# Performance work log

Measured on AMD Instinct MI355X. Metric: run time of the kernel, lower is better.

The kernel has to match this reference:

```python
import jax, jax.numpy as jnp
import numpy as np

B, C_IN, C_OUT, H, W = 128, 128, 128, 40, 40
NUM_EXPERTS, TOP_K, EXPAND = 8, 2, 2
C_HID = C_IN * EXPAND


def setup_inputs() -> dict:
    key = jax.random.key(0)
    ks = jax.random.split(key, 6)
    x = jax.random.normal(ks[0], (B, C_IN, H, W), dtype=jnp.float32)
    weights = jax.random.uniform(ks[1], (B, TOP_K), dtype=jnp.float32)
    indices = jax.random.randint(ks[2], (B, TOP_K), 0, NUM_EXPERTS, dtype=jnp.int64)
    # per-expert 1x1 conv params: expand -> SiLU -> project
    W1 = jax.random.normal(ks[3], (NUM_EXPERTS, C_HID, C_IN), dtype=jnp.float32) * (1.0 / np.sqrt(C_IN))
    b1 = jnp.zeros((NUM_EXPERTS, C_HID), dtype=jnp.float32)
    W2 = jax.random.normal(ks[4], (NUM_EXPERTS, C_OUT, C_HID), dtype=jnp.float32) * (1.0 / np.sqrt(C_HID))
    b2 = jnp.zeros((NUM_EXPERTS, C_OUT), dtype=jnp.float32)
    return {"x": x, "weights": weights, "indices": indices,
            "W1": W1, "b1": b1, "W2": W2, "b2": b2}


def reference(x, weights, indices, W1, b1, W2, b2):
    # Combine top-k gate weights per (batch, expert): duplicate expert picks sum,
    # exactly matching the original's per-expert gather + weighted index_add_.
    Bn = x.shape[0]
    E = W1.shape[0]
    gate = jnp.zeros((Bn, E), dtype=x.dtype).at[jnp.arange(Bn)[:, None], indices].add(weights)  # [B, E]
    out = jnp.zeros((Bn, W2.shape[1]) + x.shape[2:], dtype=x.dtype)
    for e in range(E):  # fixed small expert loop
        h = jax.nn.silu(jnp.einsum('bchw,oc->bohw', x, W1[e]) + b1[e][None, :, None, None])
        y = jnp.einsum('bchw,oc->bohw', h, W2[e]) + b2[e][None, :, None, None]
        out = out + y * gate[:, e][:, None, None, None]
    return out
```

## Files before the change

### kernel.cpp

```cpp
#include <hip/hip_runtime.h>

#define CIN   128
#define CHID  256
#define COUT  128
#define HWPX  1600

typedef __attribute__((ext_vector_type(8))) short bf16x8;
typedef __attribute__((ext_vector_type(4))) float f32x4;

__device__ __forceinline__ unsigned short f2bf(float f) {
  unsigned int u = __builtin_bit_cast(unsigned int, f);
  u += 0x7FFFu + ((u >> 16) & 1u);
  return (unsigned short)(u >> 16);
}
__device__ __forceinline__ unsigned int pack_bf2(float a, float b) {
  return (unsigned int)f2bf(a) | ((unsigned int)f2bf(b) << 16);
}
__device__ __forceinline__ unsigned int silu_gate_pk(float a, float b, float g) {
  const float ea = __builtin_amdgcn_exp2f(a * -1.442695041f);
  const float eb = __builtin_amdgcn_exp2f(b * -1.442695041f);
  const float sa = g * a * __builtin_amdgcn_rcpf(1.0f + ea);
  const float sb = g * b * __builtin_amdgcn_rcpf(1.0f + eb);
  return pack_bf2(sa, sb);
}

__global__ __launch_bounds__(256) void convert_w_kernel(
    const float* __restrict__ W1, const float* __restrict__ W2,
    unsigned short* __restrict__ W1c, unsigned short* __restrict__ W2c) {
  const int i    = blockIdx.x * 256 + threadIdx.x;
  const int j    = i & 7;
  const int lane = (i >> 3) & 63;
  const int r16  = lane & 15;
  const int q    = lane >> 4;
  {
    const int half = (i >> 9) & 1;
    const int ks   = (i >> 10) & 3;
    const int grp  = (i >> 12) & 7;
    const int e    = i >> 15;
    const int ch   = grp * 32 + ((r16 >> 2) << 3) + (r16 & 3) + (half << 2);
    const int c    = ks * 4 + q;
    W1c[i] = f2bf(W1[(e * CHID + ch) * CIN + c * 8 + j]);
  }
  {
    const int mt  = (i >> 9) & 7;
    const int grp = (i >> 12) & 7;
    const int e   = i >> 15;
    const int co  = mt * 16 + r16;
    W2c[i] = f2bf(W2[(e * COUT + co) * CHID + grp * 32 + q * 8 + j]);
  }
}

__global__ __launch_bounds__(256, 2) void moe_kernel(
    const float* __restrict__ x, const float* __restrict__ wts,
    const int* __restrict__ idx, const unsigned short* __restrict__ W1,
    const float* __restrict__ b1, const unsigned short* __restrict__ W2,
    const float* __restrict__ b2, float* __restrict__ out) {
  __shared__ __align__(16) unsigned short lds[32768];

  const int tid  = threadIdx.x;
  const int wave = tid >> 6;
  const int lane = tid & 63;
  const int q    = lane >> 4;
  const int r16  = lane & 15;

  const int  b    = blockIdx.x / 7;
  const int  t4   = blockIdx.x % 7;
  const int  tile = t4 * 4 + wave;
  if (tile >= 25) return;
  const int  px0  = tile * 64;

  unsigned short* xw = &lds[wave * 8192];

  {
    const float* xb = x + (long)b * CIN * HWPX + px0 + lane;
#pragma unroll 4
    for (int c = 0; c < 16; ++c) {
      float v[8];
#pragma unroll
      for (int jj = 0; jj < 8; ++jj) v[jj] = xb[(long)(c * 8 + jj) * HWPX];
      union { bf16x8 w; unsigned int u[4]; } t;
#pragma unroll
      for (int d = 0; d < 4; ++d) t.u[d] = pack_bf2(v[2 * d], v[2 * d + 1]);
      const int slot = (c + lane) & 15;
      *reinterpret_cast<bf16x8*>(&xw[(lane * 16 + slot) * 8]) = t.w;
    }
  }

  const int   e0 = __builtin_amdgcn_readfirstlane(idx[b * 2 + 0]);
  const int   e1 = __builtin_amdgcn_readfirstlane(idx[b * 2 + 1]);
  const float g0 = wts[b * 2 + 0], g1 = wts[b * 2 + 1];

  f32x4 accO[8][4];
#pragma unroll
  for (int mt = 0; mt < 8; ++mt)
#pragma unroll
    for (int nt = 0; nt < 4; ++nt) accO[mt][nt] = (f32x4){0.f, 0.f, 0.f, 0.f};

  const int lane8 = lane * 8;

  for (int gs = 0; gs < 16; ++gs) {
    const int   slot = gs >> 3;
    const int   grp  = gs & 7;
    const int   e    = slot ? e1 : e0;
    const float g    = slot ? g1 : g0;
    const unsigned short* w1s = W1 + ((long)(e * 8 + grp) << 12);
    const unsigned short* w2s = W2 + ((long)(e * 8 + grp) << 12);

    f32x4 aA[4], aB[4];
#pragma unroll
    for (int nt = 0; nt < 4; ++nt) {
      aA[nt] = (f32x4){0.f, 0.f, 0.f, 0.f};
      aB[nt] = (f32x4){0.f, 0.f, 0.f, 0.f};
    }
#pragma unroll
    for (int ks = 0; ks < 4; ++ks) {
      const bf16x8 w0 = *reinterpret_cast<const bf16x8*>(
          &w1s[(ks * 2 + 0) * 512 + lane8]);
      const bf16x8 w1v = *reinterpret_cast<const bf16x8*>(
          &w1s[(ks * 2 + 1) * 512 + lane8]);
#pragma unroll
      for (int nt = 0; nt < 4; ++nt) {
        const int px = nt * 16 + r16;
        const bf16x8 xf = *reinterpret_cast<const bf16x8*>(
            &xw[(px * 16 + ((ks * 4 + q + px) & 15)) * 8]);
        aA[nt] = __builtin_amdgcn_mfma_f32_16x16x32_bf16(w0, xf, aA[nt], 0, 0, 0);
        aB[nt] = __builtin_amdgcn_mfma_f32_16x16x32_bf16(w1v, xf, aB[nt], 0, 0, 0);
      }
    }

    const float* b1e = b1 + e * CHID + grp * 32;
    const f32x4 bA = *reinterpret_cast<const f32x4*>(&b1e[q * 8]);
    const f32x4 bB = *reinterpret_cast<const f32x4*>(&b1e[q * 8 + 4]);
    union { bf16x8 v; unsigned int u[4]; } h[4];
#pragma unroll
    for (int nt = 0; nt < 4; ++nt) {
      h[nt].u[0] = silu_gate_pk(aA[nt][0] + bA[0], aA[nt][1] + bA[1], g);
      h[nt].u[1] = silu_gate_pk(aA[nt][2] + bA[2], aA[nt][3] + bA[3], g);
      h[nt].u[2] = silu_gate_pk(aB[nt][0] + bB[0], aB[nt][1] + bB[1], g);
      h[nt].u[3] = silu_gate_pk(aB[nt][2] + bB[2], aB[nt][3] + bB[3], g);
    }

#pragma unroll
    for (int mt = 0; mt < 8; ++mt) {
      const bf16x8 w2v = *reinterpret_cast<const bf16x8*>(
          &w2s[mt * 512 + lane8]);
#pragma unroll
      for (int nt = 0; nt < 4; ++nt)
        accO[mt][nt] = __builtin_amdgcn_mfma_f32_16x16x32_bf16(w2v, h[nt].v, accO[mt][nt], 0, 0, 0);
    }
  }

  float* eb = reinterpret_cast<float*>(xw);
  const float* b2e0 = b2 + e0 * COUT;
  const float* b2e1 = b2 + e1 * COUT;
  const int  coR   = lane >> 2;
  const int  qtr   = lane & 3;
  const long orow0 = (long)b * COUT * HWPX + px0 + qtr * 16;
#pragma unroll
  for (int mt = 0; mt < 8; ++mt) {
    const int coW = q * 4;
    const f32x4 bias = g0 * (*reinterpret_cast<const f32x4*>(&b2e0[mt * 16 + coW])) +
                       g1 * (*reinterpret_cast<const f32x4*>(&b2e1[mt * 16 + coW]));
#pragma unroll
    for (int nt = 0; nt < 4; ++nt) {
      const f32x4 v = accO[mt][nt] + bias;
#pragma unroll
      for (int rr = 0; rr < 4; ++rr)
        eb[(coW + rr) * 68 + nt * 16 + r16] = v[rr];
    }
    {
      const long orow = orow0 + (long)(mt * 16 + coR) * HWPX;
#pragma unroll
      for (int i4 = 0; i4 < 4; ++i4) {
        const float4 ov = *reinterpret_cast<const float4*>(
            &eb[coR * 68 + qtr * 16 + i4 * 4]);
        *reinterpret_cast<float4*>(&out[orow + i4 * 4]) = ov;
      }
    }
  }
}

extern "C" void kernel_launch(void* const* d_in, const int* in_sizes, int n_in,
                              void* d_out, int out_size, void* d_ws, size_t ws_size,
                              hipStream_t stream) {
  const float* x   = (const float*)d_in[0];
  const float* wts = (const float*)d_in[1];
  const int*   idx = (const int*)d_in[2];
  const float* W1  = (const float*)d_in[3];
  const float* b1  = (const float*)d_in[4];
  const float* W2  = (const float*)d_in[5];
  const float* b2  = (const float*)d_in[6];
  float* out = (float*)d_out;

  unsigned short* W1c = (unsigned short*)d_ws;
  unsigned short* W2c = (unsigned short*)d_ws + (8 * CHID * CIN);

  convert_w_kernel<<<262144 / 256, 256, 0, stream>>>(W1, W2, W1c, W2c);
  moe_kernel<<<128 * 7, 256, 0, stream>>>(x, wts, idx, W1c, b1, W2c, b2, out);
}
```

Measured before the change: 314.1 us.

## Pre-convert x to bf16 tiles and double-buffer them into LDS via async loads

Adds a pre-pass that converts x to bf16 in a swizzled tile layout inside the weight-conversion kernel. The main kernel becomes persistent per batch, with 32-pixel tiles per wave, and each wave prefetches its next x tile into LDS with global_load_lds double buffering. The goal is to take the strided fp32 x gather and conversion off the MFMA kernel's critical path and to overlap tile loads with compute. In exchange, bf16 x makes an extra round trip through workspace memory, and smaller pixel tiles reuse each weight fragment less. The old path is kept as a fallback when the workspace is too small.

```diff
diff --git a/kernel.cpp b/kernel.cpp
--- a/kernel.cpp
+++ b/kernel.cpp
@@ -4,6 +4,8 @@
 #define CHID  256
 #define COUT  128
 #define HWPX  1600
+#define NT    50
+#define TPX   32
 
 typedef __attribute__((ext_vector_type(8))) short bf16x8;
 typedef __attribute__((ext_vector_type(4))) float f32x4;
@@ -24,10 +26,52 @@
   return pack_bf2(sa, sb);
 }
 
-__global__ __launch_bounds__(256) void convert_w_kernel(
-    const float* __restrict__ W1, const float* __restrict__ W2,
-    unsigned short* __restrict__ W1c, unsigned short* __restrict__ W2c) {
-  const int i    = blockIdx.x * 256 + threadIdx.x;
+__device__ __forceinline__ void stage_tile(const unsigned short* g,
+                                           unsigned short* l, int lane) {
+#pragma unroll
+  for (int k = 0; k < 8; ++k)
+    __builtin_amdgcn_global_load_lds(
+        (const __attribute__((address_space(1))) unsigned int*)(g + (k * 64 + lane) * 8),
+        (__attribute__((address_space(3))) unsigned int*)(l + k * 512),
+        16, 0, 0);
+}
+
+__global__ __launch_bounds__(256) void convert_kernel(
+    const float* __restrict__ x, const float* __restrict__ W1,
+    const float* __restrict__ W2, unsigned short* __restrict__ W1c,
+    unsigned short* __restrict__ W2c, unsigned short* __restrict__ xbf,
+    int do_x) {
+  __shared__ __align__(16) unsigned short xl[4][4096];
+  const int bid = blockIdx.x;
+  if (do_x && bid < 1664) {
+    const int wave = threadIdx.x >> 6, lane = threadIdx.x & 63;
+    const int b = bid / 13, blk = bid % 13;
+    const int tile = blk * 4 + wave;
+    if (tile >= NT) return;
+    const int p = lane & 31, h = lane >> 5;
+    const float* xr = x + (long)b * CIN * HWPX + tile * TPX + p;
+    unsigned short* w = &xl[wave][0];
+#pragma unroll
+    for (int c = 0; c < 8; ++c) {
+      const int cc = c * 2 + h;
+      float v[8];
+#pragma unroll
+      for (int jj = 0; jj < 8; ++jj) v[jj] = xr[(long)(cc * 8 + jj) * HWPX];
+      union { bf16x8 t; unsigned int u[4]; } t;
+#pragma unroll
+      for (int d = 0; d < 4; ++d) t.u[d] = pack_bf2(v[2 * d], v[2 * d + 1]);
+      const int slot = (cc + p) & 15;
+      *reinterpret_cast<bf16x8*>(&w[(p * 16 + slot) * 8]) = t.t;
+    }
+    uint4* dst = reinterpret_cast<uint4*>(xbf + ((long)b * NT + tile) * 4096);
+    const uint4* src = reinterpret_cast<const uint4*>(w);
+#pragma unroll
+    for (int k = 0; k < 8; ++k) dst[k * 64 + lane] = src[k * 64 + lane];
+    return;
+  }
+  const int wb = do_x ? (bid - 1664) : bid;
+  if (wb >= 1024) return;
+  const int i    = wb * 256 + threadIdx.x;
   const int j    = i & 7;
   const int lane = (i >> 3) & 63;
   const int r16  = lane & 15;
@@ -50,27 +94,147 @@
   }
 }
 
-__global__ __launch_bounds__(256, 2) void moe_kernel(
+__global__ __launch_bounds__(256, 2) void moe_kernel_v3(
+    const unsigned short* __restrict__ xbf, const float* __restrict__ wts,
+    const int* __restrict__ idx, const unsigned short* __restrict__ W1,
+    const float* __restrict__ b1, const unsigned short* __restrict__ W2,
+    const float* __restrict__ b2, float* __restrict__ out) {
+  __shared__ __align__(16) unsigned short lds[4][2][4096];
+
+  const int tid  = threadIdx.x;
+  const int wave = tid >> 6;
+  const int lane = tid & 63;
+  const int q    = lane >> 4;
+  const int r16  = lane & 15;
+
+  const int b    = blockIdx.x >> 2;
+  const int slot = (blockIdx.x & 3) * 4 + wave;
+  const int n    = (slot < 2) ? 4 : 3;
+
+  const int   e0 = __builtin_amdgcn_readfirstlane(idx[b * 2 + 0]);
+  const int   e1 = __builtin_amdgcn_readfirstlane(idx[b * 2 + 1]);
+  const float g0 = wts[b * 2 + 0], g1 = wts[b * 2 + 1];
+
+  const unsigned short* xb = xbf + (long)b * NT * 4096;
+  const int lane8 = lane * 8;
+
+  stage_tile(xb + (long)slot * 4096, &lds[wave][0][0], lane);
+
+  for (int i = 0; i < n; ++i) {
+    asm volatile("s_waitcnt vmcnt(0)" ::: "memory");
+    __builtin_amdgcn_sched_barrier(0);
+    if (i + 1 < n)
+      stage_tile(xb + (long)(slot + 16 * (i + 1)) * 4096,
+                 &lds[wave][(i + 1) & 1][0], lane);
+
+    unsigned short* xw = &lds[wave][i & 1][0];
+
+    f32x4 accO[8][2];
+#pragma unroll
+    for (int mt = 0; mt < 8; ++mt)
+#pragma unroll
+      for (int nt = 0; nt < 2; ++nt) accO[mt][nt] = (f32x4){0.f, 0.f, 0.f, 0.f};
+
+#pragma unroll
+    for (int gs = 0; gs < 16; ++gs) {
+      const int   sl  = gs >> 3;
+      const int   grp = gs & 7;
+      const int   e   = sl ? e1 : e0;
+      const float g   = sl ? g1 : g0;
+      const unsigned short* w1s = W1 + ((long)(e * 8 + grp) << 12);
+      const unsigned short* w2s = W2 + ((long)(e * 8 + grp) << 12);
+
+      f32x4 aA[2], aB[2];
+#pragma unroll
+      for (int nt = 0; nt < 2; ++nt) {
+        aA[nt] = (f32x4){0.f, 0.f, 0.f, 0.f};
+        aB[nt] = (f32x4){0.f, 0.f, 0.f, 0.f};
+      }
+#pragma unroll
+      for (int ks = 0; ks < 4; ++ks) {
+        const bf16x8 w0 = *reinterpret_cast<const bf16x8*>(
+            &w1s[(ks * 2 + 0) * 512 + lane8]);
+        const bf16x8 w1v = *reinterpret_cast<const bf16x8*>(
+            &w1s[(ks * 2 + 1) * 512 + lane8]);
+#pragma unroll
+        for (int nt = 0; nt < 2; ++nt) {
+          const int px = nt * 16 + r16;
+          const bf16x8 xf = *reinterpret_cast<const bf16x8*>(
+              &xw[(px * 16 + ((ks * 4 + q + px) & 15)) * 8]);
+          aA[nt] = __builtin_amdgcn_mfma_f32_16x16x32_bf16(w0, xf, aA[nt], 0, 0, 0);
+          aB[nt] = __builtin_amdgcn_mfma_f32_16x16x32_bf16(w1v, xf, aB[nt], 0, 0, 0);
+        }
+      }
+
+      const float* b1e = b1 + e * CHID + grp * 32;
+      const f32x4 bA = *reinterpret_cast<const f32x4*>(&b1e[q * 8]);
+      const f32x4 bB = *reinterpret_cast<const f32x4*>(&b1e[q * 8 + 4]);
+      union { bf16x8 v; unsigned int u[4]; } h[2];
+#pragma unroll
+      for (int nt = 0; nt < 2; ++nt) {
+        h[nt].u[0] = silu_gate_pk(aA[nt][0] + bA[0], aA[nt][1] + bA[1], g);
+        h[nt].u[1] = silu_gate_pk(aA[nt][2] + bA[2], aA[nt][3] + bA[3], g);
+        h[nt].u[2] = silu_gate_pk(aB[nt][0] + bB[0], aB[nt][1] + bB[1], g);
+        h[nt].u[3] = silu_gate_pk(aB[nt][2] + bB[2], aB[nt][3] + bB[3], g);
+      }
+
+#pragma unroll
+      for (int mt = 0; mt < 8; ++mt) {
+        const bf16x8 w2v = *reinterpret_cast<const bf16x8*>(
+            &w2s[mt * 512 + lane8]);
+#pragma unroll
+        for (int nt = 0; nt < 2; ++nt)
+          accO[mt][nt] = __builtin_amdgcn_mfma_f32_16x16x32_bf16(w2v, h[nt].v, accO[mt][nt], 0, 0, 0);
+      }
+    }
+
+    float* eb = reinterpret_cast<float*>(xw);
+    const float* b2e0 = b2 + e0 * COUT;
+    const float* b2e1 = b2 + e1 * COUT;
+    const int  coR  = lane >> 2;
+    const int  qtr  = lane & 3;
+    const long px0  = (long)(slot + 16 * i) * TPX;
+    const long obase = (long)b * COUT * HWPX + px0;
+#pragma unroll
+    for (int mt = 0; mt < 8; ++mt) {
+      const int coW = q * 4;
+      const f32x4 bias = g0 * (*reinterpret_cast<const f32x4*>(&b2e0[mt * 16 + coW])) +
+                         g1 * (*reinterpret_cast<const f32x4*>(&b2e1[mt * 16 + coW]));
+#pragma unroll
+      for (int nt = 0; nt < 2; ++nt) {
+        const f32x4 v = accO[mt][nt] + bias;
+#pragma unroll
+        for (int rr = 0; rr < 4; ++rr)
+          eb[(coW + rr) * 36 + nt * 16 + r16] = v[rr];
+      }
+      const long orow = obase + (long)(mt * 16 + coR) * HWPX;
+#pragma unroll
+      for (int k = 0; k < 2; ++k) {
+        const float4 ov = *reinterpret_cast<const float4*>(
+            &eb[coR * 36 + k * 16 + qtr * 4]);
+        *reinterpret_cast<float4*>(&out[orow + k * 16 + qtr * 4]) = ov;
+      }
+    }
+  }
+}
+
+__global__ __launch_bounds__(256, 2) void moe_kernel_v2(
     const float* __restrict__ x, const float* __restrict__ wts,
     const int* __restrict__ idx, const unsigned short* __restrict__ W1,
     const float* __restrict__ b1, const unsigned short* __restrict__ W2,
     const float* __restrict__ b2, float* __restrict__ out) {
   __shared__ __align__(16) unsigned short lds[32768];
-
   const int tid  = threadIdx.x;
   const int wave = tid >> 6;
   const int lane = tid & 63;
   const int q    = lane >> 4;
   const int r16  = lane & 15;
-
   const int  b    = blockIdx.x / 7;
   const int  t4   = blockIdx.x % 7;
   const int  tile = t4 * 4 + wave;
   if (tile >= 25) return;
   const int  px0  = tile * 64;
-
   unsigned short* xw = &lds[wave * 8192];
-
   {
     const float* xb = x + (long)b * CIN * HWPX + px0 + lane;
 #pragma unroll 4
@@ -85,27 +249,22 @@
       *reinterpret_cast<bf16x8*>(&xw[(lane * 16 + slot) * 8]) = t.w;
     }
   }
-
   const int   e0 = __builtin_amdgcn_readfirstlane(idx[b * 2 + 0]);
   const int   e1 = __builtin_amdgcn_readfirstlane(idx[b * 2 + 1]);
   const float g0 = wts[b * 2 + 0], g1 = wts[b * 2 + 1];
-
   f32x4 accO[8][4];
 #pragma unroll
   for (int mt = 0; mt < 8; ++mt)
 #pragma unroll
     for (int nt = 0; nt < 4; ++nt) accO[mt][nt] = (f32x4){0.f, 0.f, 0.f, 0.f};
-
   const int lane8 = lane * 8;
-
   for (int gs = 0; gs < 16; ++gs) {
-    const int   slot = gs >> 3;
-    const int   grp  = gs & 7;
-    const int   e    = slot ? e1 : e0;
-    const float g    = slot ? g1 : g0;
+    const int   sl  = gs >> 3;
+    const int   grp = gs & 7;
+    const int   e   = sl ? e1 : e0;
+    const float g   = sl ? g1 : g0;
     const unsigned short* w1s = W1 + ((long)(e * 8 + grp) << 12);
     const unsigned short* w2s = W2 + ((long)(e * 8 + grp) << 12);
-
     f32x4 aA[4], aB[4];
 #pragma unroll
     for (int nt = 0; nt < 4; ++nt) {
@@ -127,7 +286,6 @@
         aB[nt] = __builtin_amdgcn_mfma_f32_16x16x32_bf16(w1v, xf, aB[nt], 0, 0, 0);
       }
     }
-
     const float* b1e = b1 + e * CHID + grp * 32;
     const f32x4 bA = *reinterpret_cast<const f32x4*>(&b1e[q * 8]);
     const f32x4 bB = *reinterpret_cast<const f32x4*>(&b1e[q * 8 + 4]);
@@ -139,7 +297,6 @@
       h[nt].u[2] = silu_gate_pk(aB[nt][0] + bB[0], aB[nt][1] + bB[1], g);
       h[nt].u[3] = silu_gate_pk(aB[nt][2] + bB[2], aB[nt][3] + bB[3], g);
     }
-
 #pragma unroll
     for (int mt = 0; mt < 8; ++mt) {
       const bf16x8 w2v = *reinterpret_cast<const bf16x8*>(
@@ -149,7 +306,6 @@
         accO[mt][nt] = __builtin_amdgcn_mfma_f32_16x16x32_bf16(w2v, h[nt].v, accO[mt][nt], 0, 0, 0);
     }
   }
-
   float* eb = reinterpret_cast<float*>(xw);
   const float* b2e0 = b2 + e0 * COUT;
   const float* b2e1 = b2 + e1 * COUT;
@@ -193,8 +349,16 @@
   float* out = (float*)d_out;
 
   unsigned short* W1c = (unsigned short*)d_ws;
-  unsigned short* W2c = (unsigned short*)d_ws + (8 * CHID * CIN);
-
-  convert_w_kernel<<<262144 / 256, 256, 0, stream>>>(W1, W2, W1c, W2c);
-  moe_kernel<<<128 * 7, 256, 0, stream>>>(x, wts, idx, W1c, b1, W2c, b2, out);
-}
+  unsigned short* W2c = W1c + 8 * CHID * CIN;
+  unsigned short* xbf = W2c + 8 * CHID * CIN;
+
+  const size_t need = (size_t)2 * 8 * CHID * CIN * 2 +
+                      (size_t)128 * NT * 4096 * 2;
+  if (ws_size >= need) {
+    convert_kernel<<<1664 + 1024, 256, 0, stream>>>(x, W1, W2, W1c, W2c, xbf, 1);
+    moe_kernel_v3<<<128 * 4, 256, 0, stream>>>(xbf, wts, idx, W1c, b1, W2c, b2, out);
+  } else {
+    convert_kernel<<<1024, 256, 0, stream>>>(x, W1, W2, W1c, W2c, xbf, 0);
+    moe_kernel_v2<<<128 * 7, 256, 0, stream>>>(x, wts, idx, W1c, b1, W2c, b2, out);
+  }
+}
```

Result: slower. 471.6 us (+50.1%).

## Halve per-wave pixel tile to 32 and raise occupancy to four blocks

Applied to the files above, without the earlier changes.

Each wave now handles 32 pixels instead of 64, which halves the accumulator registers and LDS per wave. The launch bound rises to four blocks per CU and the grid grows from 7 to 13 blocks per batch to cover the 50 tiles. The x-load, epilogue staging stride and store pattern are adjusted to the new tile width. In exchange, each W1/W2 fragment loaded from global memory is reused across half as many pixels, which doubles weight traffic per pixel.

```diff
diff --git a/kernel.cpp b/kernel.cpp
--- a/kernel.cpp
+++ b/kernel.cpp
@@ -4,6 +4,7 @@
 #define CHID  256
 #define COUT  128
 #define HWPX  1600
+#define TPX   32
 
 typedef __attribute__((ext_vector_type(8))) short bf16x8;
 typedef __attribute__((ext_vector_type(4))) float f32x4;
@@ -50,12 +51,12 @@
   }
 }
 
-__global__ __launch_bounds__(256, 2) void moe_kernel(
+__global__ __launch_bounds__(256, 4) void moe_kernel(
     const float* __restrict__ x, const float* __restrict__ wts,
     const int* __restrict__ idx, const unsigned short* __restrict__ W1,
     const float* __restrict__ b1, const unsigned short* __restrict__ W2,
     const float* __restrict__ b2, float* __restrict__ out) {
-  __shared__ __align__(16) unsigned short lds[32768];
+  __shared__ __align__(16) unsigned short lds[16384];
 
   const int tid  = threadIdx.x;
   const int wave = tid >> 6;
@@ -63,52 +64,52 @@
   const int q    = lane >> 4;
   const int r16  = lane & 15;
 
-  const int  b    = blockIdx.x / 7;
-  const int  t4   = blockIdx.x % 7;
-  const int  tile = t4 * 4 + wave;
-  if (tile >= 25) return;
-  const int  px0  = tile * 64;
-
-  unsigned short* xw = &lds[wave * 8192];
-
-  {
-    const float* xb = x + (long)b * CIN * HWPX + px0 + lane;
-#pragma unroll 4
-    for (int c = 0; c < 16; ++c) {
-      float v[8];
-#pragma unroll
-      for (int jj = 0; jj < 8; ++jj) v[jj] = xb[(long)(c * 8 + jj) * HWPX];
-      union { bf16x8 w; unsigned int u[4]; } t;
-#pragma unroll
-      for (int d = 0; d < 4; ++d) t.u[d] = pack_bf2(v[2 * d], v[2 * d + 1]);
-      const int slot = (c + lane) & 15;
-      *reinterpret_cast<bf16x8*>(&xw[(lane * 16 + slot) * 8]) = t.w;
-    }
-  }
+  const int  b    = blockIdx.x / 13;
+  const int  t13  = blockIdx.x % 13;
+  const int  tile = t13 * 4 + wave;
+  if (tile >= 50) return;
+
+  unsigned short* xw = &lds[wave * 4096];
+  const int lane8 = lane * 8;
 
   const int   e0 = __builtin_amdgcn_readfirstlane(idx[b * 2 + 0]);
   const int   e1 = __builtin_amdgcn_readfirstlane(idx[b * 2 + 1]);
   const float g0 = wts[b * 2 + 0], g1 = wts[b * 2 + 1];
 
-  f32x4 accO[8][4];
+  {
+    const int p = lane & 31, hh = lane >> 5;
+    const float* xr = x + (long)b * CIN * HWPX + tile * TPX + p;
+#pragma unroll
+    for (int it = 0; it < 8; ++it) {
+      const int cc = it * 2 + hh;
+      float v[8];
+#pragma unroll
+      for (int jj = 0; jj < 8; ++jj) v[jj] = xr[(long)(cc * 8 + jj) * HWPX];
+      union { bf16x8 w; unsigned int u[4]; } t;
+#pragma unroll
+      for (int d = 0; d < 4; ++d) t.u[d] = pack_bf2(v[2 * d], v[2 * d + 1]);
+      const int slot = (cc + p) & 15;
+      *reinterpret_cast<bf16x8*>(&xw[(p * 16 + slot) * 8]) = t.w;
+    }
+  }
+
+  f32x4 accO[8][2];
 #pragma unroll
   for (int mt = 0; mt < 8; ++mt)
 #pragma unroll
-    for (int nt = 0; nt < 4; ++nt) accO[mt][nt] = (f32x4){0.f, 0.f, 0.f, 0.f};
-
-  const int lane8 = lane * 8;
+    for (int nt = 0; nt < 2; ++nt) accO[mt][nt] = (f32x4){0.f, 0.f, 0.f, 0.f};
 
   for (int gs = 0; gs < 16; ++gs) {
-    const int   slot = gs >> 3;
-    const int   grp  = gs & 7;
-    const int   e    = slot ? e1 : e0;
-    const float g    = slot ? g1 : g0;
+    const int   sl  = gs >> 3;
+    const int   grp = gs & 7;
+    const int   e   = sl ? e1 : e0;
+    const float g   = sl ? g1 : g0;
     const unsigned short* w1s = W1 + ((long)(e * 8 + grp) << 12);
     const unsigned short* w2s = W2 + ((long)(e * 8 + grp) << 12);
 
-    f32x4 aA[4], aB[4];
-#pragma unroll
-    for (int nt = 0; nt < 4; ++nt) {
+    f32x4 aA[2], aB[2];
+#pragma unroll
+    for (int nt = 0; nt < 2; ++nt) {
       aA[nt] = (f32x4){0.f, 0.f, 0.f, 0.f};
       aB[nt] = (f32x4){0.f, 0.f, 0.f, 0.f};
     }
@@ -119,7 +120,7 @@
       const bf16x8 w1v = *reinterpret_cast<const bf16x8*>(
           &w1s[(ks * 2 + 1) * 512 + lane8]);
 #pragma unroll
-      for (int nt = 0; nt < 4; ++nt) {
+      for (int nt = 0; nt < 2; ++nt) {
         const int px = nt * 16 + r16;
         const bf16x8 xf = *reinterpret_cast<const bf16x8*>(
             &xw[(px * 16 + ((ks * 4 + q + px) & 15)) * 8]);
@@ -131,9 +132,9 @@
     const float* b1e = b1 + e * CHID + grp * 32;
     const f32x4 bA = *reinterpret_cast<const f32x4*>(&b1e[q * 8]);
     const f32x4 bB = *reinterpret_cast<const f32x4*>(&b1e[q * 8 + 4]);
-    union { bf16x8 v; unsigned int u[4]; } h[4];
-#pragma unroll
-    for (int nt = 0; nt < 4; ++nt) {
+    union { bf16x8 v; unsigned int u[4]; } h[2];
+#pragma unroll
+    for (int nt = 0; nt < 2; ++nt) {
       h[nt].u[0] = silu_gate_pk(aA[nt][0] + bA[0], aA[nt][1] + bA[1], g);
       h[nt].u[1] = silu_gate_pk(aA[nt][2] + bA[2], aA[nt][3] + bA[3], g);
       h[nt].u[2] = silu_gate_pk(aB[nt][0] + bB[0], aB[nt][1] + bB[1], g);
@@ -145,7 +146,7 @@
       const bf16x8 w2v = *reinterpret_cast<const bf16x8*>(
           &w2s[mt * 512 + lane8]);
 #pragma unroll
-      for (int nt = 0; nt < 4; ++nt)
+      for (int nt = 0; nt < 2; ++nt)
         accO[mt][nt] = __builtin_amdgcn_mfma_f32_16x16x32_bf16(w2v, h[nt].v, accO[mt][nt], 0, 0, 0);
     }
   }
@@ -155,26 +156,26 @@
   const float* b2e1 = b2 + e1 * COUT;
   const int  coR   = lane >> 2;
   const int  qtr   = lane & 3;
-  const long orow0 = (long)b * COUT * HWPX + px0 + qtr * 16;
+  const long obase = (long)b * COUT * HWPX + (long)tile * TPX;
 #pragma unroll
   for (int mt = 0; mt < 8; ++mt) {
     const int coW = q * 4;
     const f32x4 bias = g0 * (*reinterpret_cast<const f32x4*>(&b2e0[mt * 16 + coW])) +
                        g1 * (*reinterpret_cast<const f32x4*>(&b2e1[mt * 16 + coW]));
 #pragma unroll
-    for (int nt = 0; nt < 4; ++nt) {
+    for (int nt = 0; nt < 2; ++nt) {
       const f32x4 v = accO[mt][nt] + bias;
 #pragma unroll
       for (int rr = 0; rr < 4; ++rr)
-        eb[(coW + rr) * 68 + nt * 16 + r16] = v[rr];
+        eb[(coW + rr) * 36 + nt * 16 + r16] = v[rr];
     }
     {
-      const long orow = orow0 + (long)(mt * 16 + coR) * HWPX;
-#pragma unroll
-      for (int i4 = 0; i4 < 4; ++i4) {
+      const long orow = obase + (long)(mt * 16 + coR) * HWPX;
+#pragma unroll
+      for (int k = 0; k < 2; ++k) {
         const float4 ov = *reinterpret_cast<const float4*>(
-            &eb[coR * 68 + qtr * 16 + i4 * 4]);
-        *reinterpret_cast<float4*>(&out[orow + i4 * 4]) = ov;
+            &eb[coR * 36 + k * 16 + qtr * 4]);
+        *reinterpret_cast<float4*>(&out[orow + k * 16 + qtr * 4]) = ov;
       }
     }
   }
@@ -196,5 +197,5 @@
   unsigned short* W2c = (unsigned short*)d_ws + (8 * CHID * CIN);
 
   convert_w_kernel<<<262144 / 256, 256, 0, stream>>>(W1, W2, W1c, W2c);
-  moe_kernel<<<128 * 7, 256, 0, stream>>>(x, wts, idx, W1c, b1, W2c, b2, out);
-}
+  moe_kernel<<<128 * 13, 256, 0, stream>>>(x, wts, idx, W1c, b1, W2c, b2, out);
+}
```

Result: no change. 314.7 us (+0.2%).
